# Kernel tuning notes

Measured on AMD Instinct MI355X. Metric: run time of the kernel, lower is better.

## Reference

```python
import jax, jax.numpy as jnp
import numpy as np

B = 4096          # batch_size
D_EMB = 16        # per-side embedding dim (embed_to_from width = 2*D_EMB)
D_HIGH = 784      # flattened high-dim feature size
NSR = 5           # negative_sample_rate
A = 1.576943      # UMAP _a
B_PARAM = 0.8950608  # UMAP _b
REPULSION = 1.0
EPS = 1e-4
GLOBAL_LOSS = 0.5
TOTAL_STEPS = 1000
BATCH_COUNT = 500  # fixed step for deterministic alpha/beta
WARMUP = int(0.05 * TOTAL_STEPS)


def _safe_sqrt(sq):
    # sqrt with zero (not NaN) gradient at 0, matching zero-distance pairs
    safe = jnp.where(sq > 0, sq, 1.0)
    return jnp.where(sq > 0, jnp.sqrt(safe), 0.0)


def _pairwise_dist(x):
    # ||x_i - x_j|| via gram trick; avoids materializing [N,N,D]
    sq = jnp.sum(x * x, axis=1)                      # [N]
    gram = x @ x.T                                   # [N,N]
    d2 = sq[:, None] + sq[None, :] - 2.0 * gram
    return _safe_sqrt(jnp.maximum(d2, 0.0))


def _umap_ce_loss(embed_to_from, perm):
    e_to, e_from = jnp.split(embed_to_from, 2, axis=1)   # [B, D_EMB] each
    neg_to = jnp.repeat(e_to, NSR, axis=0)               # [B*NSR, D_EMB]
    repeat_neg = jnp.repeat(e_from, NSR, axis=0)
    neg_from = repeat_neg[perm]                          # shuffled negatives
    d_pos = _safe_sqrt(jnp.sum((e_to - e_from) ** 2, axis=1))
    d_neg = _safe_sqrt(jnp.sum((neg_to - neg_from) ** 2, axis=1))
    dist = jnp.concatenate([d_pos, d_neg], axis=0)       # [B*(1+NSR)]
    p_dist = 1.0 / (1.0 + A * dist ** (2.0 * B_PARAM))
    p_graph = jnp.concatenate([jnp.ones(B, p_dist.dtype), jnp.zeros(B * NSR, p_dist.dtype)])
    attraction = -p_graph * jnp.log(jnp.clip(p_dist, EPS, 1.0))
    repellant = -(1.0 - p_graph) * jnp.log(jnp.clip(1.0 - p_dist, EPS, 1.0)) * REPULSION
    return jnp.mean(attraction + repellant)


def _global_feature_loss(embed_to_from, to_x):
    e_to = embed_to_from[:, :D_EMB]
    to_x = to_x.reshape(to_x.shape[0], -1)
    high_dis = _pairwise_dist(to_x)     # [N,N]
    low_dis = _pairwise_dist(e_to)      # [N,N]
    # row-wise pearson correlation between high_dis and low_dis
    h = high_dis - jnp.mean(high_dis, axis=1, keepdims=True)
    l = low_dis - jnp.mean(low_dis, axis=1, keepdims=True)
    num = jnp.sum(h * l, axis=1)
    den = jnp.sqrt(jnp.sum(h * h, axis=1)) * jnp.sqrt(jnp.sum(l * l, axis=1))
    corr = jnp.mean(num / den)
    return -corr


def _alpha_beta():
    if BATCH_COUNT >= WARMUP:
        if BATCH_COUNT <= 0.9 * TOTAL_STEPS:
            beta = max(0.0, GLOBAL_LOSS * (1 - BATCH_COUNT / (TOTAL_STEPS - WARMUP * 4)) ** 2)
        else:
            beta = 0.0
        alpha = max(0.0, 1 - beta)
    else:
        alpha = 0.0
        beta = GLOBAL_LOSS
    return alpha, beta


def setup_inputs() -> dict:
    key = jax.random.key(0)
    k1, k2, k3 = jax.random.split(key, 3)
    embed_to_from = jax.random.normal(k1, (B, 2 * D_EMB), dtype=jnp.float32)
    placeholder = jax.random.normal(k2, (B, D_HIGH), dtype=jnp.float32)
    perm = jax.random.permutation(k3, B * NSR).astype(jnp.int32)
    return {"embed_to_from": embed_to_from, "placeholder": placeholder, "perm": perm}


def reference(embed_to_from, placeholder, perm):
    loss = _umap_ce_loss(embed_to_from, perm)
    loss_g = _global_feature_loss(embed_to_from, placeholder)
    alpha, beta = _alpha_beta()
    return alpha * loss + beta * loss_g
```

## Files before the change

kernel.cpp:

```cpp
#include <hip/hip_runtime.h>
#include <hip/hip_bf16.h>
#include <math.h>

#define NB    4096
#define DH    784
#define KX8   832
#define NSR   5
#define NNEG  (NB*NSR)
#define NTOT  (NB + NNEG)

#define A_CONST 1.576943f
#define PEXP    1.7901216f
#define EPS_C   1.0e-4f
#define ALPHA_C 0.9296875f
#define BETA_C  0.0703125f

#define NSLOT 64
#define SLAB  (NB * NSLOT)
#define NBLK  528
#define BUFB  8192

typedef __hip_bfloat16 bf16;
typedef short bf16x8 __attribute__((ext_vector_type(8)));
typedef float f32x4  __attribute__((ext_vector_type(4)));
typedef long long2v __attribute__((ext_vector_type(2)));

#define WS_XF8    0
#define WS_EBF    3407872
#define WS_SQX    3670016
#define WS_SQE    3686400
#define WS_STATSP 3702784
#define WS_UPART  8945664
#define WS_CPART  8946048
#define WS_CNT    8946304

__device__ __forceinline__ void gl2lds16(const void* g, void* l) {
    __builtin_amdgcn_global_load_lds(
        (const __attribute__((address_space(1))) unsigned int*)g,
        (__attribute__((address_space(3))) unsigned int*)l,
        16, 0, 0);
}

__global__ void prep_fused(const float* __restrict__ X, const float* __restrict__ emb,
                           const int* __restrict__ perm, unsigned char* __restrict__ Xf8,
                           float* __restrict__ sqx, bf16* __restrict__ Ebf,
                           float* __restrict__ sqe, float* __restrict__ upart,
                           unsigned* __restrict__ cnt) {
    if (blockIdx.x == 0 && threadIdx.x == 0) *cnt = 0u;
    if (blockIdx.x < 1024) {
        const int wave = threadIdx.x >> 6, lane = threadIdx.x & 63;
        const int row = blockIdx.x * 4 + wave;
        const float4* xr = (const float4*)(X + (size_t)row * DH);
        int* xb = (int*)(Xf8 + (size_t)row * KX8);
        float s = 0.f;
        #pragma unroll
        for (int it = 0; it < 4; ++it) {
            const int idx = lane + it * 64;
            if (idx < 208) {
                const int c = idx >> 4, p = idx & 15;
                const int q = p >> 2, h = (p >> 1) & 1, w = p & 1;
                const int src = c * 16 + h * 8 + q * 2 + w;
                int pk = 0;
                if (src < 196) {
                    float4 v = xr[src];
                    s += v.x * v.x + v.y * v.y + v.z * v.z + v.w * v.w;
                    int lo = __builtin_amdgcn_cvt_pk_fp8_f32(v.x, v.y, 0, false);
                    pk = __builtin_amdgcn_cvt_pk_fp8_f32(v.z, v.w, lo, true);
                }
                xb[idx] = pk;
            }
        }
        #pragma unroll
        for (int off = 32; off; off >>= 1) s += __shfl_down(s, off, 64);
        if (lane == 0) sqx[row] = s;
        return;
    }
    const int ub = blockIdx.x - 1024;
    const int t = ub * 256 + threadIdx.x;
    float val = 0.f;
    if (t < NB) {
        const float4* av = (const float4*)(emb + (size_t)t * 32);
        float4 t0 = av[0], t1 = av[1], t2 = av[2], t3 = av[3];
        float4 f0 = av[4], f1 = av[5], f2 = av[6], f3 = av[7];
        bf16* eb = Ebf + (size_t)t * 32;
        union { bf16 h[4]; ushort4 u; } cv;
        #define ST4(dst, q) cv.h[0]=__float2bfloat16(q.x); cv.h[1]=__float2bfloat16(q.y); \
                            cv.h[2]=__float2bfloat16(q.z); cv.h[3]=__float2bfloat16(q.w); \
                            *(ushort4*)(dst) = cv.u;
        ST4(eb,      t0) ST4(eb + 4,  t1) ST4(eb + 8,  t2) ST4(eb + 12, t3)
        #undef ST4
        ushort4 z = {0, 0, 0, 0};
        *(ushort4*)(eb + 16) = z; *(ushort4*)(eb + 20) = z;
        *(ushort4*)(eb + 24) = z; *(ushort4*)(eb + 28) = z;
        sqe[t] = t0.x*t0.x + t0.y*t0.y + t0.z*t0.z + t0.w*t0.w
               + t1.x*t1.x + t1.y*t1.y + t1.z*t1.z + t1.w*t1.w
               + t2.x*t2.x + t2.y*t2.y + t2.z*t2.z + t2.w*t2.w
               + t3.x*t3.x + t3.y*t3.y + t3.z*t3.z + t3.w*t3.w;
        float d2 = 0.f;
        #define D2(a, b) { float4 df = {a.x-b.x, a.y-b.y, a.z-b.z, a.w-b.w}; \
                           d2 += df.x*df.x + df.y*df.y + df.z*df.z + df.w*df.w; }
        D2(t0, f0) D2(t1, f1) D2(t2, f2) D2(t3, f3)
        #undef D2
        float d = sqrtf(d2);
        float p = 1.f / (1.f + A_CONST * powf(d, PEXP));
        val = -logf(fminf(fmaxf(p, EPS_C), 1.f));
    } else if (t < NTOT) {
        const int k = t - NB;
        const int ti = k / 5;
        const int fi = perm[k] / 5;
        const float4* at = (const float4*)(emb + (size_t)ti * 32);
        const float4* bt = (const float4*)(emb + (size_t)fi * 32 + 16);
        float d2 = 0.f;
        #pragma unroll
        for (int q = 0; q < 4; ++q) {
            float4 a = at[q], b = bt[q];
            float4 df = {a.x-b.x, a.y-b.y, a.z-b.z, a.w-b.w};
            d2 += df.x*df.x + df.y*df.y + df.z*df.z + df.w*df.w;
        }
        float d = sqrtf(d2);
        float p = 1.f / (1.f + A_CONST * powf(d, PEXP));
        val = -logf(fminf(fmaxf(1.f - p, EPS_C), 1.f));
    }
    #pragma unroll
    for (int off = 32; off; off >>= 1) val += __shfl_down(val, off, 64);
    __shared__ float ps[4];
    if ((threadIdx.x & 63) == 0) ps[threadIdx.x >> 6] = val;
    __syncthreads();
    if (threadIdx.x == 0) upart[ub] = ps[0] + ps[1] + ps[2] + ps[3];
}

__global__ __launch_bounds__(256, 3) void gram_kernel(
    const unsigned char* __restrict__ Xf8, const bf16* __restrict__ Ebf,
    const float* __restrict__ sqx, const float* __restrict__ sqe,
    float* __restrict__ statsp) {
    __shared__ unsigned char As[3 * BUFB];
    __shared__ unsigned char Bs[3 * BUFB];
    __shared__ float sqxs[256];
    __shared__ float sqes[256];

    int n = (blockIdx.x & 7) * 66 + (blockIdx.x >> 3);
    int bi = 0;
    while (n >= 32 - bi) { n -= 32 - bi; ++bi; }
    const int bj = bi + n;
    const int i0 = bi * 128, j0 = bj * 128;

    const int tid  = threadIdx.x;
    const int wave = tid >> 6;
    const int lane = tid & 63;
    const int wy = wave >> 1, wx = wave & 1;
    const int quad = lane >> 4, l15 = lane & 15;

    f32x4 acc[4][4];
    #pragma unroll
    for (int a = 0; a < 4; ++a)
        #pragma unroll
        for (int b = 0; b < 4; ++b)
            acc[a][b] = (f32x4){0.f, 0.f, 0.f, 0.f};

    const int c0  = wave * 2;
    const int rA  = lane >> 2;
    const int gsb = (((lane & 3) ^ ((lane >> 3) & 3))) * 16;

    const unsigned char* gA0 = Xf8 + (size_t)(i0 + c0 * 16 + rA) * KX8 + gsb;
    const unsigned char* gA1 = Xf8 + (size_t)(i0 + c0 * 16 + 16 + rA) * KX8 + gsb;
    const unsigned char* gB0 = Xf8 + (size_t)(j0 + c0 * 16 + rA) * KX8 + gsb;
    const unsigned char* gB1 = Xf8 + (size_t)(j0 + c0 * 16 + 16 + rA) * KX8 + gsb;

    if (tid < 128) {
        sqxs[tid] = sqx[i0 + tid]; sqxs[128 + tid] = sqx[j0 + tid];
        sqes[tid] = sqe[i0 + tid]; sqes[128 + tid] = sqe[j0 + tid];
    }
    __syncthreads();

    #pragma unroll
    for (int s = 0; s < 2; ++s) {
        gl2lds16(gA0, As + s * BUFB + c0 * 1024);
        gl2lds16(gA1, As + s * BUFB + c0 * 1024 + 1024);
        gl2lds16(gB0, Bs + s * BUFB + c0 * 1024);
        gl2lds16(gB1, Bs + s * BUFB + c0 * 1024 + 1024);
        gA0 += 64; gA1 += 64; gB0 += 64; gB1 += 64;
    }

    const int key = (l15 >> 1) & 3;
    const int boX = ((quad ^ key) << 4);

    int cur = 0;
    for (int t = 0; t < 13; ++t) {
        asm volatile("s_waitcnt vmcnt(4)" ::: "memory");
        __builtin_amdgcn_s_barrier();
        const int nb = (cur + 2 * BUFB >= 3 * BUFB) ? cur - BUFB : cur + 2 * BUFB;
        if (t < 11) {
            gl2lds16(gA0, As + nb + c0 * 1024);
            gl2lds16(gA1, As + nb + c0 * 1024 + 1024);
            gl2lds16(gB0, Bs + nb + c0 * 1024);
            gl2lds16(gB1, Bs + nb + c0 * 1024 + 1024);
            gA0 += 64; gA1 += 64; gB0 += 64; gB1 += 64;
        } else if (t == 11) {
            gl2lds16((const unsigned char*)(Ebf + (size_t)(i0 + c0 * 16 + rA) * 32) + gsb,
                     As + BUFB + c0 * 1024);
            gl2lds16((const unsigned char*)(Ebf + (size_t)(i0 + c0 * 16 + 16 + rA) * 32) + gsb,
                     As + BUFB + c0 * 1024 + 1024);
            gl2lds16((const unsigned char*)(Ebf + (size_t)(j0 + c0 * 16 + rA) * 32) + gsb,
                     Bs + BUFB + c0 * 1024);
            gl2lds16((const unsigned char*)(Ebf + (size_t)(j0 + c0 * 16 + 16 + rA) * 32) + gsb,
                     Bs + BUFB + c0 * 1024 + 1024);
        }
        long2v aF[4], bF[4];
        #pragma unroll
        for (int mi = 0; mi < 4; ++mi)
            aF[mi] = *(const long2v*)&As[cur + (wy * 64 + mi * 16 + l15) * 64 + boX];
        #pragma unroll
        for (int ni = 0; ni < 4; ++ni)
            bF[ni] = *(const long2v*)&Bs[cur + (wx * 64 + ni * 16 + l15) * 64 + boX];
        #pragma unroll
        for (int mi = 0; mi < 4; ++mi)
            #pragma unroll
            for (int ni = 0; ni < 4; ++ni) {
                acc[mi][ni] = __builtin_amdgcn_mfma_f32_16x16x32_fp8_fp8(
                    aF[mi][0], bF[ni][0], acc[mi][ni], 0, 0, 0);
                acc[mi][ni] = __builtin_amdgcn_mfma_f32_16x16x32_fp8_fp8(
                    aF[mi][1], bF[ni][1], acc[mi][ni], 0, 0, 0);
            }
        cur = (cur == 2 * BUFB) ? 0 : cur + BUFB;
    }
    asm volatile("s_waitcnt vmcnt(0)" ::: "memory");
    __builtin_amdgcn_s_barrier();

    const int slot_r = bj * 2 + wx;
    const int slot_c = bi * 2 + wy;
    bf16x8 bfrE[4];
    #pragma unroll
    for (int ni = 0; ni < 4; ++ni)
        bfrE[ni] = *(const bf16x8*)&Bs[BUFB + (wx * 64 + ni * 16 + l15) * 64 + boX];
    float cH[4] = {0,0,0,0}, cH2[4] = {0,0,0,0}, cL[4] = {0,0,0,0},
          cL2[4] = {0,0,0,0}, cHL[4] = {0,0,0,0};
    #pragma unroll
    for (int mi = 0; mi < 4; ++mi) {
        bf16x8 afE = *(const bf16x8*)&As[BUFB + (wy * 64 + mi * 16 + l15) * 64 + boX];
        f32x4 aE[4];
        #pragma unroll
        for (int ni = 0; ni < 4; ++ni) {
            f32x4 z = (f32x4){0.f, 0.f, 0.f, 0.f};
            aE[ni] = __builtin_amdgcn_mfma_f32_16x16x32_bf16(afE, bfrE[ni], z, 0, 0, 0);
        }
        const int ilocb = wy * 64 + mi * 16 + quad * 4;
        float sH[4] = {0,0,0,0}, sH2[4] = {0,0,0,0}, sL[4] = {0,0,0,0},
              sL2[4] = {0,0,0,0}, sHL[4] = {0,0,0,0};
        #pragma unroll
        for (int ni = 0; ni < 4; ++ni) {
            const int jloc = wx * 64 + ni * 16 + l15;
            const int j = j0 + jloc;
            const float sqxj = sqxs[128 + jloc];
            const float sqej = sqes[128 + jloc];
            #pragma unroll
            for (int r = 0; r < 4; ++r) {
                const int iloc = ilocb + r;
                const int i = i0 + iloc;
                float H, L;
                if (i == j) { H = 0.f; L = 0.f; }
                else {
                    float d2  = sqxs[iloc] + sqxj - 2.0f * acc[mi][ni][r];
                    H = sqrtf(fmaxf(d2, 0.f));
                    float d2e = sqes[iloc] + sqej - 2.0f * aE[ni][r];
                    L = sqrtf(fmaxf(d2e, 0.f));
                }
                sH[r] += H; sH2[r] += H * H; sL[r] += L; sL2[r] += L * L; sHL[r] += H * L;
                cH[ni] += H; cH2[ni] += H * H; cL[ni] += L; cL2[ni] += L * L; cHL[ni] += H * L;
            }
        }
        #pragma unroll
        for (int r = 0; r < 4; ++r) {
            float v0 = sH[r], v1 = sH2[r], v2 = sL[r], v3 = sL2[r], v4 = sHL[r];
            #pragma unroll
            for (int off2 = 1; off2 < 16; off2 <<= 1) {
                v0 += __shfl_xor(v0, off2, 64);
                v1 += __shfl_xor(v1, off2, 64);
                v2 += __shfl_xor(v2, off2, 64);
                v3 += __shfl_xor(v3, off2, 64);
                v4 += __shfl_xor(v4, off2, 64);
            }
            if (l15 == 0) {
                const int i = i0 + ilocb + r;
                float* base = statsp + (size_t)slot_r * NB + i;
                base[0 * SLAB] = v0;
                base[1 * SLAB] = v1;
                base[2 * SLAB] = v2;
                base[3 * SLAB] = v3;
                base[4 * SLAB] = v4;
            }
        }
    }
    if (bi != bj) {
        #pragma unroll
        for (int ni = 0; ni < 4; ++ni) {
            float v0 = cH[ni], v1 = cH2[ni], v2 = cL[ni], v3 = cL2[ni], v4 = cHL[ni];
            #pragma unroll
            for (int off2 = 16; off2 < 64; off2 <<= 1) {
                v0 += __shfl_xor(v0, off2, 64);
                v1 += __shfl_xor(v1, off2, 64);
                v2 += __shfl_xor(v2, off2, 64);
                v3 += __shfl_xor(v3, off2, 64);
                v4 += __shfl_xor(v4, off2, 64);
            }
            if (quad == 0) {
                const int j = j0 + wx * 64 + ni * 16 + l15;
                float* base = statsp + (size_t)slot_c * NB + j;
                base[0 * SLAB] = v0;
                base[1 * SLAB] = v1;
                base[2 * SLAB] = v2;
                base[3 * SLAB] = v3;
                base[4 * SLAB] = v4;
            }
        }
    }
}

__global__ void finish1_kernel(const float* __restrict__ statsp, const float* __restrict__ upart,
                               float* __restrict__ cpart, unsigned* __restrict__ cnt,
                               float* __restrict__ out) {
    __shared__ float ps2[4][64][5];
    const int t = threadIdx.x;
    const int rloc = t & 63;
    const int sg = t >> 6;
    const int r = blockIdx.x * 64 + rloc;
    float sh = 0.f, sh2 = 0.f, sl = 0.f, sl2 = 0.f, shl = 0.f;
    for (int s = sg * 16; s < sg * 16 + 16; ++s) {
        const float* base = statsp + (size_t)s * NB + r;
        sh  += base[0 * SLAB];
        sh2 += base[1 * SLAB];
        sl  += base[2 * SLAB];
        sl2 += base[3 * SLAB];
        shl += base[4 * SLAB];
    }
    ps2[sg][rloc][0] = sh; ps2[sg][rloc][1] = sh2; ps2[sg][rloc][2] = sl;
    ps2[sg][rloc][3] = sl2; ps2[sg][rloc][4] = shl;
    __syncthreads();
    if (t < 64) {
        float a = 0.f, b = 0.f, c = 0.f, d = 0.f, e = 0.f;
        #pragma unroll
        for (int g = 0; g < 4; ++g) {
            a += ps2[g][t][0]; b += ps2[g][t][1]; c += ps2[g][t][2];
            d += ps2[g][t][3]; e += ps2[g][t][4];
        }
        const float invN = 1.0f / (float)NB;
        float num = e - a * c * invN;
        float vh  = fmaxf(b - a * a * invN, 0.f);
        float vl  = fmaxf(d - c * c * invN, 0.f);
        float local = num / (sqrtf(vh) * sqrtf(vl));
        #pragma unroll
        for (int off = 32; off; off >>= 1) local += __shfl_down(local, off, 64);
        if (t == 0) cpart[blockIdx.x] = local;
    }
    __shared__ int lastFlag;
    if (t == 0) {
        __threadfence();
        unsigned prev = atomicAdd(cnt, 1u);
        lastFlag = (prev == 63u);
    }
    __syncthreads();
    if (lastFlag) {
        __threadfence();
        float v = 0.f;
        if (t < 64) v += cpart[t] * (-BETA_C / (float)NB);
        if (t < 96) v += upart[t] * (ALPHA_C / (float)NTOT);
        #pragma unroll
        for (int off = 32; off; off >>= 1) v += __shfl_down(v, off, 64);
        __shared__ float fin[4];
        if ((t & 63) == 0) fin[t >> 6] = v;
        __syncthreads();
        if (t == 0) out[0] = fin[0] + fin[1] + fin[2] + fin[3];
    }
}

extern "C" void kernel_launch(void* const* d_in, const int* in_sizes, int n_in,
                              void* d_out, int out_size, void* d_ws, size_t ws_size,
                              hipStream_t stream) {
    const float* emb  = (const float*)d_in[0];
    const float* ph   = (const float*)d_in[1];
    const int*   perm = (const int*)d_in[2];
    float* out = (float*)d_out;

    char* ws = (char*)d_ws;
    unsigned char* Xf8 = (unsigned char*)(ws + WS_XF8);
    bf16*  Ebf    = (bf16*) (ws + WS_EBF);
    float* sqx    = (float*)(ws + WS_SQX);
    float* sqe    = (float*)(ws + WS_SQE);
    float* statsp = (float*)(ws + WS_STATSP);
    float* upart  = (float*)(ws + WS_UPART);
    float* cpart  = (float*)(ws + WS_CPART);
    unsigned* cnt = (unsigned*)(ws + WS_CNT);

    prep_fused<<<1120, 256, 0, stream>>>(ph, emb, perm, Xf8, sqx, Ebf, sqe, upart, cnt);
    gram_kernel<<<NBLK, 256, 0, stream>>>(Xf8, Ebf, sqx, sqe, statsp);
    finish1_kernel<<<64, 256, 0, stream>>>(statsp, upart, cpart, cnt, out);
}
```

Before: 119.9 us.

## Use 8 waves per gram block and reduce row/column stats through LDS

The gram kernel now runs 512 threads, 8 waves in a 4x2 grid, each owning a 32x64 sub-tile, which halves the per-wave accumulators. Global-to-LDS loads are spread across the extra waves. The row and column statistic reductions move from cross-lane shuffles to LDS scratch that reuses the staging buffer, followed by a cooperative sum. The goal is more resident waves to hide latency and fewer shuffles, at the cost of extra barriers and LDS traffic in the epilogue.

```diff
diff --git a/kernel.cpp b/kernel.cpp
--- a/kernel.cpp
+++ b/kernel.cpp
@@ -23,6 +23,7 @@
 typedef __hip_bfloat16 bf16;
 typedef short bf16x8 __attribute__((ext_vector_type(8)));
 typedef float f32x4  __attribute__((ext_vector_type(4)));
+typedef float f32x2  __attribute__((ext_vector_type(2)));
 typedef long long2v __attribute__((ext_vector_type(2)));
 
 #define WS_XF8    0
@@ -129,14 +130,16 @@
     if (threadIdx.x == 0) upart[ub] = ps[0] + ps[1] + ps[2] + ps[3];
 }
 
-__global__ __launch_bounds__(256, 3) void gram_kernel(
+__global__ __launch_bounds__(512, 4) void gram_kernel(
     const unsigned char* __restrict__ Xf8, const bf16* __restrict__ Ebf,
     const float* __restrict__ sqx, const float* __restrict__ sqe,
     float* __restrict__ statsp) {
-    __shared__ unsigned char As[3 * BUFB];
-    __shared__ unsigned char Bs[3 * BUFB];
-    __shared__ float sqxs[256];
-    __shared__ float sqes[256];
+    __shared__ __align__(16) unsigned char smem[51200];
+    unsigned char* As = smem;
+    unsigned char* Bs = smem + 3 * BUFB;
+    float* sqxs = (float*)(smem + 49152);
+    float* sqes = (float*)(smem + 50176);
+    float* scr  = (float*)smem;
 
     int n = (blockIdx.x & 7) * 66 + (blockIdx.x >> 3);
     int bi = 0;
@@ -150,21 +153,17 @@
     const int wy = wave >> 1, wx = wave & 1;
     const int quad = lane >> 4, l15 = lane & 15;
 
-    f32x4 acc[4][4];
-    #pragma unroll
-    for (int a = 0; a < 4; ++a)
+    f32x4 acc[2][4];
+    #pragma unroll
+    for (int a = 0; a < 2; ++a)
         #pragma unroll
         for (int b = 0; b < 4; ++b)
             acc[a][b] = (f32x4){0.f, 0.f, 0.f, 0.f};
 
-    const int c0  = wave * 2;
     const int rA  = lane >> 2;
     const int gsb = (((lane & 3) ^ ((lane >> 3) & 3))) * 16;
-
-    const unsigned char* gA0 = Xf8 + (size_t)(i0 + c0 * 16 + rA) * KX8 + gsb;
-    const unsigned char* gA1 = Xf8 + (size_t)(i0 + c0 * 16 + 16 + rA) * KX8 + gsb;
-    const unsigned char* gB0 = Xf8 + (size_t)(j0 + c0 * 16 + rA) * KX8 + gsb;
-    const unsigned char* gB1 = Xf8 + (size_t)(j0 + c0 * 16 + 16 + rA) * KX8 + gsb;
+    const unsigned char* gA = Xf8 + (size_t)(i0 + wave * 16 + rA) * KX8 + gsb;
+    const unsigned char* gB = Xf8 + (size_t)(j0 + wave * 16 + rA) * KX8 + gsb;
 
     if (tid < 128) {
         sqxs[tid] = sqx[i0 + tid]; sqxs[128 + tid] = sqx[j0 + tid];
@@ -174,11 +173,9 @@
 
     #pragma unroll
     for (int s = 0; s < 2; ++s) {
-        gl2lds16(gA0, As + s * BUFB + c0 * 1024);
-        gl2lds16(gA1, As + s * BUFB + c0 * 1024 + 1024);
-        gl2lds16(gB0, Bs + s * BUFB + c0 * 1024);
-        gl2lds16(gB1, Bs + s * BUFB + c0 * 1024 + 1024);
-        gA0 += 64; gA1 += 64; gB0 += 64; gB1 += 64;
+        gl2lds16(gA, As + s * BUFB + wave * 1024);
+        gl2lds16(gB, Bs + s * BUFB + wave * 1024);
+        gA += 64; gB += 64;
     }
 
     const int key = (l15 >> 1) & 3;
@@ -186,34 +183,28 @@
 
     int cur = 0;
     for (int t = 0; t < 13; ++t) {
-        asm volatile("s_waitcnt vmcnt(4)" ::: "memory");
+        asm volatile("s_waitcnt vmcnt(2)" ::: "memory");
         __builtin_amdgcn_s_barrier();
         const int nb = (cur + 2 * BUFB >= 3 * BUFB) ? cur - BUFB : cur + 2 * BUFB;
         if (t < 11) {
-            gl2lds16(gA0, As + nb + c0 * 1024);
-            gl2lds16(gA1, As + nb + c0 * 1024 + 1024);
-            gl2lds16(gB0, Bs + nb + c0 * 1024);
-            gl2lds16(gB1, Bs + nb + c0 * 1024 + 1024);
-            gA0 += 64; gA1 += 64; gB0 += 64; gB1 += 64;
+            gl2lds16(gA, As + nb + wave * 1024);
+            gl2lds16(gB, Bs + nb + wave * 1024);
+            gA += 64; gB += 64;
         } else if (t == 11) {
-            gl2lds16((const unsigned char*)(Ebf + (size_t)(i0 + c0 * 16 + rA) * 32) + gsb,
-                     As + BUFB + c0 * 1024);
-            gl2lds16((const unsigned char*)(Ebf + (size_t)(i0 + c0 * 16 + 16 + rA) * 32) + gsb,
-                     As + BUFB + c0 * 1024 + 1024);
-            gl2lds16((const unsigned char*)(Ebf + (size_t)(j0 + c0 * 16 + rA) * 32) + gsb,
-                     Bs + BUFB + c0 * 1024);
-            gl2lds16((const unsigned char*)(Ebf + (size_t)(j0 + c0 * 16 + 16 + rA) * 32) + gsb,
-                     Bs + BUFB + c0 * 1024 + 1024);
-        }
-        long2v aF[4], bF[4];
-        #pragma unroll
-        for (int mi = 0; mi < 4; ++mi)
-            aF[mi] = *(const long2v*)&As[cur + (wy * 64 + mi * 16 + l15) * 64 + boX];
+            gl2lds16((const unsigned char*)(Ebf + (size_t)(i0 + wave * 16 + rA) * 32) + gsb,
+                     As + BUFB + wave * 1024);
+            gl2lds16((const unsigned char*)(Ebf + (size_t)(j0 + wave * 16 + rA) * 32) + gsb,
+                     Bs + BUFB + wave * 1024);
+        }
+        long2v aF[2], bF[4];
+        #pragma unroll
+        for (int mi = 0; mi < 2; ++mi)
+            aF[mi] = *(const long2v*)&As[cur + (wy * 32 + mi * 16 + l15) * 64 + boX];
         #pragma unroll
         for (int ni = 0; ni < 4; ++ni)
             bF[ni] = *(const long2v*)&Bs[cur + (wx * 64 + ni * 16 + l15) * 64 + boX];
         #pragma unroll
-        for (int mi = 0; mi < 4; ++mi)
+        for (int mi = 0; mi < 2; ++mi)
             #pragma unroll
             for (int ni = 0; ni < 4; ++ni) {
                 acc[mi][ni] = __builtin_amdgcn_mfma_f32_16x16x32_fp8_fp8(
@@ -226,91 +217,99 @@
     asm volatile("s_waitcnt vmcnt(0)" ::: "memory");
     __builtin_amdgcn_s_barrier();
 
-    const int slot_r = bj * 2 + wx;
-    const int slot_c = bi * 2 + wy;
-    bf16x8 bfrE[4];
+    bf16x8 afE[2], bfrE[4];
+    #pragma unroll
+    for (int mi = 0; mi < 2; ++mi)
+        afE[mi] = *(const bf16x8*)&As[BUFB + (wy * 32 + mi * 16 + l15) * 64 + boX];
     #pragma unroll
     for (int ni = 0; ni < 4; ++ni)
         bfrE[ni] = *(const bf16x8*)&Bs[BUFB + (wx * 64 + ni * 16 + l15) * 64 + boX];
-    float cH[4] = {0,0,0,0}, cH2[4] = {0,0,0,0}, cL[4] = {0,0,0,0},
-          cL2[4] = {0,0,0,0}, cHL[4] = {0,0,0,0};
-    #pragma unroll
-    for (int mi = 0; mi < 4; ++mi) {
-        bf16x8 afE = *(const bf16x8*)&As[BUFB + (wy * 64 + mi * 16 + l15) * 64 + boX];
+    float sqxj[4], sqej[4];
+    #pragma unroll
+    for (int ni = 0; ni < 4; ++ni) {
+        const int jl = wx * 64 + ni * 16 + l15;
+        sqxj[ni] = sqxs[128 + jl]; sqej[ni] = sqes[128 + jl];
+    }
+    __syncthreads();
+
+    float cst[4][5];
+    #pragma unroll
+    for (int ni = 0; ni < 4; ++ni)
+        #pragma unroll
+        for (int c = 0; c < 5; ++c) cst[ni][c] = 0.f;
+
+    #pragma unroll
+    for (int mi = 0; mi < 2; ++mi) {
         f32x4 aE[4];
         #pragma unroll
         for (int ni = 0; ni < 4; ++ni) {
             f32x4 z = (f32x4){0.f, 0.f, 0.f, 0.f};
-            aE[ni] = __builtin_amdgcn_mfma_f32_16x16x32_bf16(afE, bfrE[ni], z, 0, 0, 0);
-        }
-        const int ilocb = wy * 64 + mi * 16 + quad * 4;
-        float sH[4] = {0,0,0,0}, sH2[4] = {0,0,0,0}, sL[4] = {0,0,0,0},
-              sL2[4] = {0,0,0,0}, sHL[4] = {0,0,0,0};
+            aE[ni] = __builtin_amdgcn_mfma_f32_16x16x32_bf16(afE[mi], bfrE[ni], z, 0, 0, 0);
+        }
+        const int ilb = wy * 32 + mi * 16 + quad * 4;
+        float sqxi[4], sqei[4];
+        #pragma unroll
+        for (int r = 0; r < 4; ++r) { sqxi[r] = sqxs[ilb + r]; sqei[r] = sqes[ilb + r]; }
+        float rs[5][4];
+        #pragma unroll
+        for (int c = 0; c < 5; ++c)
+            #pragma unroll
+            for (int r = 0; r < 4; ++r) rs[c][r] = 0.f;
         #pragma unroll
         for (int ni = 0; ni < 4; ++ni) {
-            const int jloc = wx * 64 + ni * 16 + l15;
-            const int j = j0 + jloc;
-            const float sqxj = sqxs[128 + jloc];
-            const float sqej = sqes[128 + jloc];
+            const int j = j0 + wx * 64 + ni * 16 + l15;
             #pragma unroll
             for (int r = 0; r < 4; ++r) {
-                const int iloc = ilocb + r;
-                const int i = i0 + iloc;
+                const int i = i0 + ilb + r;
                 float H, L;
                 if (i == j) { H = 0.f; L = 0.f; }
                 else {
-                    float d2  = sqxs[iloc] + sqxj - 2.0f * acc[mi][ni][r];
+                    float d2  = sqxi[r] + sqxj[ni] - 2.0f * acc[mi][ni][r];
                     H = sqrtf(fmaxf(d2, 0.f));
-                    float d2e = sqes[iloc] + sqej - 2.0f * aE[ni][r];
+                    float d2e = sqei[r] + sqej[ni] - 2.0f * aE[ni][r];
                     L = sqrtf(fmaxf(d2e, 0.f));
                 }
-                sH[r] += H; sH2[r] += H * H; sL[r] += L; sL2[r] += L * L; sHL[r] += H * L;
-                cH[ni] += H; cH2[ni] += H * H; cL[ni] += L; cL2[ni] += L * L; cHL[ni] += H * L;
+                rs[0][r] += H; rs[1][r] += H * H; rs[2][r] += L;
+                rs[3][r] += L * L; rs[4][r] += H * L;
+                cst[ni][0] += H; cst[ni][1] += H * H; cst[ni][2] += L;
+                cst[ni][3] += L * L; cst[ni][4] += H * L;
             }
         }
         #pragma unroll
-        for (int r = 0; r < 4; ++r) {
-            float v0 = sH[r], v1 = sH2[r], v2 = sL[r], v3 = sL2[r], v4 = sHL[r];
-            #pragma unroll
-            for (int off2 = 1; off2 < 16; off2 <<= 1) {
-                v0 += __shfl_xor(v0, off2, 64);
-                v1 += __shfl_xor(v1, off2, 64);
-                v2 += __shfl_xor(v2, off2, 64);
-                v3 += __shfl_xor(v3, off2, 64);
-                v4 += __shfl_xor(v4, off2, 64);
-            }
-            if (l15 == 0) {
-                const int i = i0 + ilocb + r;
-                float* base = statsp + (size_t)slot_r * NB + i;
-                base[0 * SLAB] = v0;
-                base[1 * SLAB] = v1;
-                base[2 * SLAB] = v2;
-                base[3 * SLAB] = v3;
-                base[4 * SLAB] = v4;
-            }
-        }
-    }
+        for (int c = 0; c < 5; ++c)
+            #pragma unroll
+            for (int r = 0; r < 4; ++r)
+                scr[(size_t)((((wx * 5 + c) << 6) + (wy << 4) + (quad << 2) + r)) * 18 + l15]
+                    = rs[c][r];
+        __syncthreads();
+        for (int o = tid; o < 640; o += 512) {
+            const int wxo = (o >= 320) ? 1 : 0;
+            const int rem = o - wxo * 320;
+            const int c = rem >> 6, li = rem & 63;
+            const float* p = scr + (size_t)(((wxo * 5 + c) << 6) + li) * 18;
+            float s = 0.f;
+            #pragma unroll
+            for (int k = 0; k < 16; k += 2) { f32x2 v = *(const f32x2*)&p[k]; s += v.x + v.y; }
+            const int iloc = ((li >> 4) << 5) + mi * 16 + (li & 15);
+            statsp[(size_t)c * SLAB + (size_t)(bj * 2 + wxo) * NB + (i0 + iloc)] = s;
+        }
+        __syncthreads();
+    }
+
     if (bi != bj) {
         #pragma unroll
         for (int ni = 0; ni < 4; ++ni) {
-            float v0 = cH[ni], v1 = cH2[ni], v2 = cL[ni], v3 = cL2[ni], v4 = cHL[ni];
-            #pragma unroll
-            for (int off2 = 16; off2 < 64; off2 <<= 1) {
-                v0 += __shfl_xor(v0, off2, 64);
-                v1 += __shfl_xor(v1, off2, 64);
-                v2 += __shfl_xor(v2, off2, 64);
-                v3 += __shfl_xor(v3, off2, 64);
-                v4 += __shfl_xor(v4, off2, 64);
-            }
-            if (quad == 0) {
-                const int j = j0 + wx * 64 + ni * 16 + l15;
-                float* base = statsp + (size_t)slot_c * NB + j;
-                base[0 * SLAB] = v0;
-                base[1 * SLAB] = v1;
-                base[2 * SLAB] = v2;
-                base[3 * SLAB] = v3;
-                base[4 * SLAB] = v4;
-            }
+            const int jl = wx * 64 + ni * 16 + l15;
+            #pragma unroll
+            for (int c = 0; c < 5; ++c)
+                scr[(size_t)(c * 128 + jl) * 17 + (wy << 2) + quad] = cst[ni][c];
+        }
+        __syncthreads();
+        for (int o = tid; o < 1280; o += 512) {
+            const int c = o >> 8, h = (o >> 7) & 1, j = o & 127;
+            const float* p = scr + (size_t)(c * 128 + j) * 17 + h * 8;
+            float s = ((p[0] + p[1]) + (p[2] + p[3])) + ((p[4] + p[5]) + (p[6] + p[7]));
+            statsp[(size_t)c * SLAB + (size_t)(bi * 2 + h) * NB + (j0 + j)] = s;
         }
     }
 }
@@ -391,6 +390,6 @@
     unsigned* cnt = (unsigned*)(ws + WS_CNT);
 
     prep_fused<<<1120, 256, 0, stream>>>(ph, emb, perm, Xf8, sqx, Ebf, sqe, upart, cnt);
-    gram_kernel<<<NBLK, 256, 0, stream>>>(Xf8, Ebf, sqx, sqe, statsp);
+    gram_kernel<<<NBLK, 512, 0, stream>>>(Xf8, Ebf, sqx, sqe, statsp);
     finish1_kernel<<<64, 256, 0, stream>>>(statsp, upart, cpart, cnt, out);
 }
```

Result: no change. 121.2 us (+1.1%).
